# Kernel optimization log

Hardware: AMD Instinct MI355X
Metric: run time of the kernel (lower is better)

Reference implementation:

```python
import jax, jax.numpy as jnp
import numpy as np

D = 1024
H = 16
HD = D // H
FF = 4096
EPS = 1e-5


def setup_inputs() -> dict:
    key = jax.random.key(0)
    ks = jax.random.split(key, 12)
    s = lambda fan_in: 1.0 / np.sqrt(fan_in)
    return {
        "x": jax.random.normal(ks[0], (8, 1024, D), dtype=jnp.float32),
        "ln1_g": jnp.ones((D,), jnp.float32),
        "ln1_b": jnp.zeros((D,), jnp.float32),
        "ln2_g": jnp.ones((D,), jnp.float32),
        "ln2_b": jnp.zeros((D,), jnp.float32),
        "qkv_w": jax.random.uniform(ks[1], (3 * D, D), jnp.float32, -s(D), s(D)),
        "q_bias": jnp.zeros((D,), jnp.float32),
        "v_bias": jnp.zeros((D,), jnp.float32),
        "proj_w": jax.random.uniform(ks[2], (D, D), jnp.float32, -s(D), s(D)),
        "proj_b": jnp.zeros((D,), jnp.float32),
        "fc1_w": jax.random.uniform(ks[3], (FF, D), jnp.float32, -s(D), s(D)),
        "fc1_b": jnp.zeros((FF,), jnp.float32),
        "fc2_w": jax.random.uniform(ks[4], (D, FF), jnp.float32, -s(FF), s(FF)),
        "fc2_b": jnp.zeros((D,), jnp.float32),
    }


def _layernorm(x, g, b):
    mu = jnp.mean(x, axis=-1, keepdims=True)
    var = jnp.mean(jnp.square(x - mu), axis=-1, keepdims=True)
    return (x - mu) * jax.lax.rsqrt(var + EPS) * g + b


def reference(x, ln1_g, ln1_b, ln2_g, ln2_b, qkv_w, q_bias, v_bias,
              proj_w, proj_b, fc1_w, fc1_b, fc2_w, fc2_b):
    b, n, d = x.shape
    scale = HD ** (-0.5)
    # --- attention branch ---
    h = _layernorm(x, ln1_g, ln1_b)
    qkv_bias = jnp.concatenate([q_bias, jnp.zeros_like(v_bias), v_bias])
    qkv = h @ qkv_w.T + qkv_bias  # [b, n, 3d]
    qkv = qkv.reshape(b, n, 3, H, HD).transpose(2, 0, 3, 1, 4)  # [3, b, h, n, hd]
    q, k, v = qkv[0], qkv[1], qkv[2]
    attn = jnp.einsum("bhnd,bhmd->bhnm", q * scale, k)
    attn = jax.nn.softmax(attn, axis=-1)
    o = jnp.einsum("bhnm,bhmd->bhnd", attn, v)
    o = o.transpose(0, 2, 1, 3).reshape(b, n, d)
    x = x + (o @ proj_w.T + proj_b)
    # --- mlp branch ---
    h = _layernorm(x, ln2_g, ln2_b)
    h = jax.nn.gelu(h @ fc1_w.T + fc1_b, approximate=False)
    x = x + (h @ fc2_w.T + fc2_b)
    return x
```

## Files before the change

kernel.cpp:

```cpp
#include <hip/hip_runtime.h>
#include <hip/hip_bf16.h>


typedef __attribute__((ext_vector_type(8))) short short8;
typedef __attribute__((ext_vector_type(4))) float floatx4;

__device__ __forceinline__ unsigned short f2bf(float f) {
  union { __hip_bfloat16 h; unsigned short u; } cv;
  cv.h = __float2bfloat16(f);
  return cv.u;
}

__device__ __forceinline__ float fast_exp2(float x) {
  return __builtin_amdgcn_exp2f(x);
}

__device__ __forceinline__ void async_ld16(const void* g, void* l) {
  __builtin_amdgcn_global_load_lds(
      (const __attribute__((address_space(1))) unsigned int*)g,
      (__attribute__((address_space(3))) unsigned int*)l, 16, 0, 0);
}

__global__ __launch_bounds__(256) void cvt_bf16(const float* __restrict__ in,
                                                unsigned short* __restrict__ out) {
  const long i = ((long)blockIdx.x * 256 + threadIdx.x) * 4;
  const float4 v = *(const float4*)(in + i);
  ushort4 o;
  o.x = f2bf(v.x); o.y = f2bf(v.y); o.z = f2bf(v.z); o.w = f2bf(v.w);
  *(ushort4*)(out + i) = o;
}

__global__ __launch_bounds__(256) void ln_bf16(const float* __restrict__ x,
                                               const float* __restrict__ g,
                                               const float* __restrict__ b,
                                               unsigned short* __restrict__ out) {
  const int row = blockIdx.x;
  const int tid = threadIdx.x;
  const float4 v = ((const float4*)(x + (long)row * 1024))[tid];
  float s = v.x + v.y + v.z + v.w;
  float ss = v.x * v.x + v.y * v.y + v.z * v.z + v.w * v.w;
#pragma unroll
  for (int off = 1; off < 64; off <<= 1) {
    s += __shfl_xor(s, off);
    ss += __shfl_xor(ss, off);
  }
  __shared__ float red[8];
  const int wave = tid >> 6, lane = tid & 63;
  if (lane == 0) { red[wave] = s; red[4 + wave] = ss; }
  __syncthreads();
  if (tid == 0) {
    red[0] = red[0] + red[1] + red[2] + red[3];
    red[4] = red[4] + red[5] + red[6] + red[7];
  }
  __syncthreads();
  const float mu = red[0] * (1.f / 1024.f);
  const float var = red[4] * (1.f / 1024.f) - mu * mu;
  const float rstd = rsqrtf(var + 1e-5f);
  const int c = tid * 4;
  ushort4 o;
  o.x = f2bf((v.x - mu) * rstd * g[c + 0] + b[c + 0]);
  o.y = f2bf((v.y - mu) * rstd * g[c + 1] + b[c + 1]);
  o.z = f2bf((v.z - mu) * rstd * g[c + 2] + b[c + 2]);
  o.w = f2bf((v.w - mu) * rstd * g[c + 3] + b[c + 3]);
  ((ushort4*)(out + (long)row * 1024))[tid] = o;
}

#define BM 128
#define BN 128
#define BK 32

template <int MODE>
__global__ __launch_bounds__(256) void gemm_bt(
    const unsigned short* __restrict__ A, const unsigned short* __restrict__ B,
    int M, int N, int Kd,
    const float* __restrict__ b0, const float* __restrict__ b1,
    const float* __restrict__ resid,
    void* __restrict__ out0, void* __restrict__ out1, void* __restrict__ out2) {
  __shared__ unsigned short lA[BM * BK];
  __shared__ unsigned short lB[BN * BK];
  const int tid = threadIdx.x;
  const int wave = tid >> 6, lane = tid & 63;
  const int l16 = lane & 15, quad = lane >> 4;
  const int wr = wave >> 1, wc = wave & 1;
  const long m0 = (long)blockIdx.y * BM;
  const long n0 = (long)blockIdx.x * BN;

  floatx4 acc[4][4];
#pragma unroll
  for (int i = 0; i < 4; i++)
#pragma unroll
    for (int j = 0; j < 4; j++) acc[i][j] = (floatx4){0.f, 0.f, 0.f, 0.f};

  for (int k0 = 0; k0 < Kd; k0 += BK) {
#pragma unroll
    for (int j = 0; j < 2; j++) {
      const int c = j * 256 + tid;
      const int row = c >> 2, kc = c & 3;
      async_ld16(A + (m0 + row) * Kd + k0 + kc * 8,
                 (char*)lA + (wave * 64 + j * 256) * 16);
      async_ld16(B + (n0 + row) * Kd + k0 + kc * 8,
                 (char*)lB + (wave * 64 + j * 256) * 16);
    }
    __syncthreads();
    short8 af[4], bfv[4];
#pragma unroll
    for (int mi = 0; mi < 4; mi++)
      af[mi] = *(const short8*)(lA + (wr * 64 + mi * 16 + l16) * BK + quad * 8);
#pragma unroll
    for (int ni = 0; ni < 4; ni++)
      bfv[ni] = *(const short8*)(lB + (wc * 64 + ni * 16 + l16) * BK + quad * 8);
#pragma unroll
    for (int mi = 0; mi < 4; mi++)
#pragma unroll
      for (int ni = 0; ni < 4; ni++)
        acc[mi][ni] = __builtin_amdgcn_mfma_f32_16x16x32_bf16(
            af[mi], bfv[ni], acc[mi][ni], 0, 0, 0);
    __syncthreads();
  }

#pragma unroll
  for (int mi = 0; mi < 4; mi++) {
    const long rbase = m0 + wr * 64 + mi * 16 + quad * 4;
#pragma unroll
    for (int ni = 0; ni < 4; ni++) {
      const long cg = n0 + wc * 64 + ni * 16 + l16;
#pragma unroll
      for (int reg = 0; reg < 4; reg++) {
        const long rr = rbase + reg;
        const float val = acc[mi][ni][reg];
        if (MODE == 0) {
          const int which = (int)(cg >> 10);
          const int col = (int)(cg & 1023);
          const int bidx = (int)(rr >> 10), t = (int)(rr & 1023);
          const int head = col >> 6, hd = col & 63;
          const long bh = bidx * 16 + head;
          if (which == 0) {
            ((unsigned short*)out0)[(bh * 1024 + t) * 64 + hd] =
                f2bf((val + b0[col]) * 0.1803368801111244f);
          } else if (which == 1) {
            ((unsigned short*)out1)[(bh * 1024 + t) * 64 + hd] = f2bf(val);
          } else {
            ((unsigned short*)out2)[(bh * 64 + hd) * 1024 + t] =
                f2bf(val + b1[col]);
          }
        } else if (MODE == 1) {
          const long idx = rr * N + cg;
          ((float*)out0)[idx] = resid[idx] + val + b0[cg];
        } else {
          const float u = val + b0[cg];
          const float gl = 0.5f * u * (1.0f + erff(u * 0.70710678118f));
          ((unsigned short*)out0)[rr * N + cg] = f2bf(gl);
        }
      }
    }
  }
}

__global__ __launch_bounds__(256) void attn(const unsigned short* __restrict__ Q,
                                            const unsigned short* __restrict__ Kc,
                                            const unsigned short* __restrict__ Vt,
                                            unsigned short* __restrict__ O) {
  __shared__ unsigned short lK[2][2048];
  __shared__ unsigned short lV[2][2048];
  __shared__ float P[4][2][16][34];
  const int tid = threadIdx.x;
  const int wave = tid >> 6, lane = tid & 63;
  const int l16 = lane & 15, quad = lane >> 4;
  const int bh = blockIdx.y;
  const int q0 = blockIdx.x * 128 + wave * 32;
  const unsigned short* Qb = Q + ((long)bh * 1024 + q0) * 64;
  const unsigned short* Kb = Kc + (long)bh * 65536;
  const unsigned short* Vb = Vt + (long)bh * 65536;

  short8 qf[2][2];
#pragma unroll
  for (int t = 0; t < 2; t++)
#pragma unroll
    for (int h = 0; h < 2; h++)
      qf[t][h] = *(const short8*)(Qb + (t * 16 + l16) * 64 + h * 32 + quad * 8);

  const int kr = tid >> 3;
  const int kc = (tid & 7) ^ (kr & 7);
  const unsigned short* kSrc = Kb + kr * 64 + kc * 8;
  const int vr = tid >> 2;
  const int vc = (tid & 3) ^ (vr & 3) ^ ((vr >> 2) & 3);
  const unsigned short* vSrc = Vb + vr * 1024 + vc * 8;

  floatx4 oacc[2][4];
#pragma unroll
  for (int t = 0; t < 2; t++)
#pragma unroll
    for (int u = 0; u < 4; u++) oacc[t][u] = (floatx4){0.f, 0.f, 0.f, 0.f};
  float lrun[2][4] = {{0.f, 0.f, 0.f, 0.f}, {0.f, 0.f, 0.f, 0.f}};

  async_ld16(kSrc, (char*)&lK[0][0] + wave * 1024);
  async_ld16(vSrc, (char*)&lV[0][0] + wave * 1024);

  const int vca = quad ^ (l16 & 3) ^ ((l16 >> 2) & 3);

  for (int ks = 0; ks < 1024; ks += 32) {
    const int buf = (ks >> 5) & 1;
    __syncthreads();
    const int kn = ks + 32;
    if (kn < 1024) {
      async_ld16(kSrc + kn * 64, (char*)&lK[buf ^ 1][0] + wave * 1024);
      async_ld16(vSrc + kn,      (char*)&lV[buf ^ 1][0] + wave * 1024);
    }
    short8 kf[2][2];
#pragma unroll
    for (int i = 0; i < 2; i++)
#pragma unroll
      for (int h = 0; h < 2; h++) {
        const int gr = (i * 16 + l16) * 8 + ((h * 4 + quad) ^ (l16 & 7));
        kf[i][h] = *(const short8*)(&lK[buf][gr * 8]);
      }
    floatx4 s[2][2];
#pragma unroll
    for (int t = 0; t < 2; t++)
#pragma unroll
      for (int i = 0; i < 2; i++) {
        const floatx4 z = {0.f, 0.f, 0.f, 0.f};
        floatx4 a = __builtin_amdgcn_mfma_f32_16x16x32_bf16(qf[t][0], kf[i][0], z, 0, 0, 0);
        s[t][i] = __builtin_amdgcn_mfma_f32_16x16x32_bf16(qf[t][1], kf[i][1], a, 0, 0, 0);
      }
#pragma unroll
    for (int t = 0; t < 2; t++)
#pragma unroll
      for (int r = 0; r < 4; r++) {
        const float p0 = fast_exp2(s[t][0][r]);
        const float p1 = fast_exp2(s[t][1][r]);
        lrun[t][r] += p0 + p1;
        P[wave][t][quad * 4 + r][l16] = p0;
        P[wave][t][quad * 4 + r][16 + l16] = p1;
      }
    short8 vf[4];
#pragma unroll
    for (int u = 0; u < 4; u++)
      vf[u] = *(const short8*)(&lV[buf][((u * 16 + l16) * 4 + vca) * 8]);
    short8 pf[2];
#pragma unroll
    for (int t = 0; t < 2; t++) {
      const float* pr = &P[wave][t][l16][quad * 8];
      const floatx4 pa = *(const floatx4*)pr;
      const floatx4 pb = *(const floatx4*)(pr + 4);
      pf[t][0] = (short)f2bf(pa[0]); pf[t][1] = (short)f2bf(pa[1]);
      pf[t][2] = (short)f2bf(pa[2]); pf[t][3] = (short)f2bf(pa[3]);
      pf[t][4] = (short)f2bf(pb[0]); pf[t][5] = (short)f2bf(pb[1]);
      pf[t][6] = (short)f2bf(pb[2]); pf[t][7] = (short)f2bf(pb[3]);
    }
#pragma unroll
    for (int t = 0; t < 2; t++)
#pragma unroll
      for (int u = 0; u < 4; u++)
        oacc[t][u] = __builtin_amdgcn_mfma_f32_16x16x32_bf16(pf[t], vf[u], oacc[t][u], 0, 0, 0);
  }

  const int b = bh >> 4, h = bh & 15;
#pragma unroll
  for (int t = 0; t < 2; t++) {
#pragma unroll
    for (int r = 0; r < 4; r++) {
      float lr = lrun[t][r];
      lr += __shfl_xor(lr, 1);
      lr += __shfl_xor(lr, 2);
      lr += __shfl_xor(lr, 4);
      lr += __shfl_xor(lr, 8);
      const float linv = 1.0f / lr;
#pragma unroll
      for (int u = 0; u < 4; u++) {
        O[((long)b * 1024 + q0 + t * 16 + quad * 4 + r) * 1024 + h * 64 + u * 16 + l16] =
            f2bf(oacc[t][u][r] * linv);
      }
    }
  }
}

extern "C" void kernel_launch(void* const* d_in, const int* in_sizes, int n_in,
                              void* d_out, int out_size, void* d_ws, size_t ws_size,
                              hipStream_t stream) {
  const float* x      = (const float*)d_in[0];
  const float* ln1_g  = (const float*)d_in[1];
  const float* ln1_b  = (const float*)d_in[2];
  const float* ln2_g  = (const float*)d_in[3];
  const float* ln2_b  = (const float*)d_in[4];
  const float* qkv_w  = (const float*)d_in[5];
  const float* q_bias = (const float*)d_in[6];
  const float* v_bias = (const float*)d_in[7];
  const float* proj_w = (const float*)d_in[8];
  const float* proj_b = (const float*)d_in[9];
  const float* fc1_w  = (const float*)d_in[10];
  const float* fc1_b  = (const float*)d_in[11];
  const float* fc2_w  = (const float*)d_in[12];
  const float* fc2_b  = (const float*)d_in[13];
  float* out = (float*)d_out;

  char* ws = (char*)d_ws;
  unsigned short* Wqkv  = (unsigned short*)(ws);
  unsigned short* Wproj = (unsigned short*)(ws + 6291456);
  unsigned short* Wfc1  = (unsigned short*)(ws + 8388608);
  unsigned short* Wfc2  = (unsigned short*)(ws + 16777216);
  float*          X1    = (float*)        (ws + 25165824);
  unsigned short* Hbuf  = (unsigned short*)(ws + 58720256);
  unsigned short* Qbuf  = (unsigned short*)(ws + 75497472);
  unsigned short* Kbuf  = (unsigned short*)(ws + 92274688);
  unsigned short* Vtbuf = (unsigned short*)(ws + 109051904);
  unsigned short* Obuf  = (unsigned short*)(ws + 125829120);
  unsigned short* ACT   = Qbuf;

  cvt_bf16<<<3072 * 1024 / 1024, 256, 0, stream>>>(qkv_w, Wqkv);
  cvt_bf16<<<1024 * 1024 / 1024, 256, 0, stream>>>(proj_w, Wproj);
  cvt_bf16<<<4096 * 1024 / 1024, 256, 0, stream>>>(fc1_w, Wfc1);
  cvt_bf16<<<4096 * 1024 / 1024, 256, 0, stream>>>(fc2_w, Wfc2);

  ln_bf16<<<8192, 256, 0, stream>>>(x, ln1_g, ln1_b, Hbuf);
  gemm_bt<0><<<dim3(24, 64), 256, 0, stream>>>(Hbuf, Wqkv, 8192, 3072, 1024,
                                               q_bias, v_bias, nullptr,
                                               Qbuf, Kbuf, Vtbuf);
  attn<<<dim3(8, 128), 256, 0, stream>>>(Qbuf, Kbuf, Vtbuf, Obuf);
  gemm_bt<1><<<dim3(8, 64), 256, 0, stream>>>(Obuf, Wproj, 8192, 1024, 1024,
                                              proj_b, nullptr, x,
                                              X1, nullptr, nullptr);
  ln_bf16<<<8192, 256, 0, stream>>>(X1, ln2_g, ln2_b, Hbuf);
  gemm_bt<2><<<dim3(32, 64), 256, 0, stream>>>(Hbuf, Wfc1, 8192, 4096, 1024,
                                               fc1_b, nullptr, nullptr,
                                               ACT, nullptr, nullptr);
  gemm_bt<1><<<dim3(8, 64), 256, 0, stream>>>(ACT, Wfc2, 8192, 1024, 4096,
                                              fc2_b, nullptr, X1,
                                              out, nullptr, nullptr);
  (void)in_sizes; (void)n_in; (void)out_size; (void)ws_size;
}
```

Before: 651.5 us.

## Double-buffer GEMM LDS tiles and remap blocks per XCD for L2 locality

The GEMM now keeps two LDS buffers and issues the async global-to-LDS loads for the next K tile before computing on the current one. This hides load latency and drops one barrier per iteration. GEMM and attention launches become 1D grids, with block IDs remapped so consecutive blocks on the same XCD share M rows or heads, aiming for better L2 reuse. The cost is double the LDS footprint, which may lower occupancy. The single barrier also relies on the async-load wait ordering being correct.

```diff
diff --git a/kernel.cpp b/kernel.cpp
--- a/kernel.cpp
+++ b/kernel.cpp
@@ -76,14 +76,23 @@
     const float* __restrict__ b0, const float* __restrict__ b1,
     const float* __restrict__ resid,
     void* __restrict__ out0, void* __restrict__ out1, void* __restrict__ out2) {
-  __shared__ unsigned short lA[BM * BK];
-  __shared__ unsigned short lB[BN * BK];
+  __shared__ unsigned short lA[2][BM * BK];
+  __shared__ unsigned short lB[2][BN * BK];
   const int tid = threadIdx.x;
   const int wave = tid >> 6, lane = tid & 63;
   const int l16 = lane & 15, quad = lane >> 4;
   const int wr = wave >> 1, wc = wave & 1;
-  const long m0 = (long)blockIdx.y * BM;
-  const long n0 = (long)blockIdx.x * BN;
+  const int bid = blockIdx.x;
+  const int xcd = bid & 7;
+  const int s = bid >> 3;
+  const long m0 = (long)(xcd * 8 + (s & 7)) * BM;
+  const long n0 = (long)(s >> 3) * BN;
+
+  const int row = tid >> 2, kc = tid & 3;
+  const unsigned short* aSrc = A + (m0 + row) * Kd + kc * 8;
+  const unsigned short* bSrc = B + (n0 + row) * Kd + kc * 8;
+  const int ldsOff0 = wave * 1024;
+  const int ldsOff1 = wave * 1024 + 4096;
 
   floatx4 acc[4][4];
 #pragma unroll
@@ -91,31 +100,34 @@
 #pragma unroll
     for (int j = 0; j < 4; j++) acc[i][j] = (floatx4){0.f, 0.f, 0.f, 0.f};
 
+  async_ld16(aSrc, (char*)&lA[0][0] + ldsOff0);
+  async_ld16(aSrc + 64 * Kd, (char*)&lA[0][0] + ldsOff1);
+  async_ld16(bSrc, (char*)&lB[0][0] + ldsOff0);
+  async_ld16(bSrc + 64 * Kd, (char*)&lB[0][0] + ldsOff1);
+
   for (int k0 = 0; k0 < Kd; k0 += BK) {
-#pragma unroll
-    for (int j = 0; j < 2; j++) {
-      const int c = j * 256 + tid;
-      const int row = c >> 2, kc = c & 3;
-      async_ld16(A + (m0 + row) * Kd + k0 + kc * 8,
-                 (char*)lA + (wave * 64 + j * 256) * 16);
-      async_ld16(B + (n0 + row) * Kd + k0 + kc * 8,
-                 (char*)lB + (wave * 64 + j * 256) * 16);
-    }
+    const int buf = (k0 >> 5) & 1;
     __syncthreads();
+    const int kn = k0 + BK;
+    if (kn < Kd) {
+      async_ld16(aSrc + kn, (char*)&lA[buf ^ 1][0] + ldsOff0);
+      async_ld16(aSrc + 64 * Kd + kn, (char*)&lA[buf ^ 1][0] + ldsOff1);
+      async_ld16(bSrc + kn, (char*)&lB[buf ^ 1][0] + ldsOff0);
+      async_ld16(bSrc + 64 * Kd + kn, (char*)&lB[buf ^ 1][0] + ldsOff1);
+    }
     short8 af[4], bfv[4];
 #pragma unroll
     for (int mi = 0; mi < 4; mi++)
-      af[mi] = *(const short8*)(lA + (wr * 64 + mi * 16 + l16) * BK + quad * 8);
+      af[mi] = *(const short8*)(&lA[buf][(wr * 64 + mi * 16 + l16) * BK + quad * 8]);
 #pragma unroll
     for (int ni = 0; ni < 4; ni++)
-      bfv[ni] = *(const short8*)(lB + (wc * 64 + ni * 16 + l16) * BK + quad * 8);
+      bfv[ni] = *(const short8*)(&lB[buf][(wc * 64 + ni * 16 + l16) * BK + quad * 8]);
 #pragma unroll
     for (int mi = 0; mi < 4; mi++)
 #pragma unroll
       for (int ni = 0; ni < 4; ni++)
         acc[mi][ni] = __builtin_amdgcn_mfma_f32_16x16x32_bf16(
             af[mi], bfv[ni], acc[mi][ni], 0, 0, 0);
-    __syncthreads();
   }
 
 #pragma unroll
@@ -166,8 +178,11 @@
   const int tid = threadIdx.x;
   const int wave = tid >> 6, lane = tid & 63;
   const int l16 = lane & 15, quad = lane >> 4;
-  const int bh = blockIdx.y;
-  const int q0 = blockIdx.x * 128 + wave * 32;
+  const int bid = blockIdx.x;
+  const int xcd = bid & 7;
+  const int sl = bid >> 3;
+  const int bh = xcd * 16 + (sl & 15);
+  const int q0 = (sl >> 4) * 128 + wave * 32;
   const unsigned short* Qb = Q + ((long)bh * 1024 + q0) * 64;
   const unsigned short* Kb = Kc + (long)bh * 65536;
   const unsigned short* Vb = Vt + (long)bh * 65536;
@@ -313,19 +328,19 @@
   cvt_bf16<<<4096 * 1024 / 1024, 256, 0, stream>>>(fc2_w, Wfc2);
 
   ln_bf16<<<8192, 256, 0, stream>>>(x, ln1_g, ln1_b, Hbuf);
-  gemm_bt<0><<<dim3(24, 64), 256, 0, stream>>>(Hbuf, Wqkv, 8192, 3072, 1024,
-                                               q_bias, v_bias, nullptr,
-                                               Qbuf, Kbuf, Vtbuf);
-  attn<<<dim3(8, 128), 256, 0, stream>>>(Qbuf, Kbuf, Vtbuf, Obuf);
-  gemm_bt<1><<<dim3(8, 64), 256, 0, stream>>>(Obuf, Wproj, 8192, 1024, 1024,
-                                              proj_b, nullptr, x,
-                                              X1, nullptr, nullptr);
+  gemm_bt<0><<<24 * 64, 256, 0, stream>>>(Hbuf, Wqkv, 8192, 3072, 1024,
+                                          q_bias, v_bias, nullptr,
+                                          Qbuf, Kbuf, Vtbuf);
+  attn<<<1024, 256, 0, stream>>>(Qbuf, Kbuf, Vtbuf, Obuf);
+  gemm_bt<1><<<8 * 64, 256, 0, stream>>>(Obuf, Wproj, 8192, 1024, 1024,
+                                         proj_b, nullptr, x,
+                                         X1, nullptr, nullptr);
   ln_bf16<<<8192, 256, 0, stream>>>(X1, ln2_g, ln2_b, Hbuf);
-  gemm_bt<2><<<dim3(32, 64), 256, 0, stream>>>(Hbuf, Wfc1, 8192, 4096, 1024,
-                                               fc1_b, nullptr, nullptr,
-                                               ACT, nullptr, nullptr);
-  gemm_bt<1><<<dim3(8, 64), 256, 0, stream>>>(ACT, Wfc2, 8192, 1024, 4096,
-                                              fc2_b, nullptr, X1,
-                                              out, nullptr, nullptr);
+  gemm_bt<2><<<32 * 64, 256, 0, stream>>>(Hbuf, Wfc1, 8192, 4096, 1024,
+                                          fc1_b, nullptr, nullptr,
+                                          ACT, nullptr, nullptr);
+  gemm_bt<1><<<8 * 64, 256, 0, stream>>>(ACT, Wfc2, 8192, 1024, 4096,
+                                         fc2_b, nullptr, X1,
+                                         out, nullptr, nullptr);
   (void)in_sizes; (void)n_in; (void)out_size; (void)ws_size;
 }
```

New measurement: 592.0 us. -9.1%, faster.
